# Kernel optimization log

Hardware: AMD Instinct MI355X
Metric: run time of the kernel (lower is better)

## Reference

```python
import jax, jax.numpy as jnp
import numpy as np

H = 23            # hidden size
NUM_LAYERS = 3
F_IN = 32         # input features
OUT = 8           # output size
B = 2048
T = 512


def _gru_dir(x_seq, w_ih, w_hh, b_ih, b_hh, reverse):
    """One direction of a GRU layer. x_seq: [T,B,in] -> [T,B,H] (time-aligned)."""
    # Precompute input-side gates for all timesteps: [T,B,3H]
    xg = jnp.einsum('tbi,gi->tbg', x_seq, w_ih) + b_ih

    def step(h, xg_t):
        hg = h @ w_hh.T + b_hh                      # [B,3H]
        r = jax.nn.sigmoid(xg_t[:, :H] + hg[:, :H])
        z = jax.nn.sigmoid(xg_t[:, H:2 * H] + hg[:, H:2 * H])
        n = jnp.tanh(xg_t[:, 2 * H:] + r * hg[:, 2 * H:])
        h_new = (1.0 - z) * n + z * h
        return h_new, h_new

    h0 = jnp.zeros((x_seq.shape[1], H), x_seq.dtype)
    _, ys = jax.lax.scan(step, h0, xg, reverse=reverse)
    return ys  # outputs aligned to original time order for both directions


def setup_inputs() -> dict:
    key = jax.random.key(0)
    ks = jax.random.split(key, 16)
    s = 1.0 / np.sqrt(H)  # PyTorch GRU default init scale

    def u(k, shape):
        return jax.random.uniform(k, shape, jnp.float32, -s, s)

    inp = {}
    inp['x'] = jax.random.normal(ks[0], (B, T, F_IN), jnp.float32)
    inp['feature_mean'] = jax.random.normal(ks[1], (F_IN,), jnp.float32) * 0.1
    # std in (0.5, 1.5): no zeros, no exact ones
    inp['feature_std'] = jax.random.uniform(ks[2], (F_IN,), jnp.float32, 0.5, 1.5)
    inp['output_mean'] = jax.random.normal(ks[3], (OUT,), jnp.float32) * 0.1
    inp['output_std'] = jax.random.uniform(ks[4], (OUT,), jnp.float32, 0.5, 1.5)

    # layer 0 params, stacked over direction [2, ...]
    inp['w_ih_l0'] = u(ks[5], (2, 3 * H, F_IN))
    inp['w_hh_l0'] = u(ks[6], (2, 3 * H, H))
    inp['b_ih_l0'] = u(ks[7], (2, 3 * H))
    inp['b_hh_l0'] = u(ks[8], (2, 3 * H))
    # layers 1..2, input size = 2H; stacked [layer, dir, ...]
    inp['w_ih_rest'] = u(ks[9], (NUM_LAYERS - 1, 2, 3 * H, 2 * H))
    inp['w_hh_rest'] = u(ks[10], (NUM_LAYERS - 1, 2, 3 * H, H))
    inp['b_ih_rest'] = u(ks[11], (NUM_LAYERS - 1, 2, 3 * H))
    inp['b_hh_rest'] = u(ks[12], (NUM_LAYERS - 1, 2, 3 * H))

    # fc: xavier_uniform for weight, pytorch default uniform for bias
    fan = OUT + 2 * H
    lim = np.sqrt(6.0 / fan)
    inp['fc_w'] = jax.random.uniform(ks[13], (OUT, 2 * H), jnp.float32, -lim, lim)
    bl = 1.0 / np.sqrt(2 * H)
    inp['fc_b'] = jax.random.uniform(ks[14], (OUT,), jnp.float32, -bl, bl)
    return inp


def reference(x, feature_mean, feature_std, output_mean, output_std,
              w_ih_l0, w_hh_l0, b_ih_l0, b_hh_l0,
              w_ih_rest, w_hh_rest, b_ih_rest, b_hh_rest,
              fc_w, fc_b):
    # feature normalization: std==0 -> 1, then zero out features where adjusted std==1
    std_adj = jnp.where(feature_std == 0.0, 1.0, feature_std)
    x = jnp.where(std_adj == 1.0, 0.0, (x - feature_mean) / std_adj)

    seq = jnp.swapaxes(x, 0, 1)  # [T,B,F] for scan over time
    for layer in range(NUM_LAYERS):
        if layer == 0:
            wih, whh, bih, bhh = w_ih_l0, w_hh_l0, b_ih_l0, b_hh_l0
        else:
            wih, whh = w_ih_rest[layer - 1], w_hh_rest[layer - 1]
            bih, bhh = b_ih_rest[layer - 1], b_hh_rest[layer - 1]
        fwd = _gru_dir(seq, wih[0], whh[0], bih[0], bhh[0], reverse=False)
        bwd = _gru_dir(seq, wih[1], whh[1], bih[1], bhh[1], reverse=True)
        seq = jnp.concatenate([fwd, bwd], axis=-1)  # [T,B,2H]

    last = seq[-1]                 # out[:, -1, :] in batch_first layout -> [B,2H]
    out = last @ fc_w.T + fc_b     # [B,OUT]
    out = out * output_std + output_mean
    return out
```

## Files before the change

### kernel.cpp

```cpp
#include <hip/hip_runtime.h>
#include <hip/hip_bf16.h>

constexpr int TT = 512, BB = 2048, NOUT = 8;
constexpr size_t DSTRIDE = (size_t)BB * TT * 24;

typedef __attribute__((ext_vector_type(8))) _Float16 f16x8;
typedef __attribute__((ext_vector_type(4))) float f32x4;
typedef __attribute__((ext_vector_type(2))) _Float16 f16x2;

__device__ __forceinline__ float sigm(float x) {
    float e = __builtin_amdgcn_exp2f(x * -1.4426950408889634f);
    return __builtin_amdgcn_rcpf(1.f + e);
}
__device__ __forceinline__ float tanh_(float x) {
    float e = __builtin_amdgcn_exp2f(x * 2.8853900817779268f);
    return __builtin_fmaf(-2.f, __builtin_amdgcn_rcpf(e + 1.f), 1.f);
}
__device__ __forceinline__ f16x2 asf16x2(unsigned v) {
    f16x2 r; __builtin_memcpy(&r, &v, 4); return r;
}
__device__ __forceinline__ f16x2 pkrtz(float a, float b) {
    auto p = __builtin_amdgcn_cvt_pkrtz(a, b);
    f16x2 r; __builtin_memcpy(&r, &p, 4); return r;
}
__device__ __forceinline__ void wbar() { __builtin_amdgcn_wave_barrier(); }

template <bool L0, bool LAST>
__global__ __launch_bounds__(256) void gru_mfma(
    const void* __restrict__ in_,
    const float* __restrict__ fmean, const float* __restrict__ fstd,
    const float* __restrict__ wih_g, const float* __restrict__ whh_g,
    const float* __restrict__ bih_g, const float* __restrict__ bhh_g,
    unsigned short* __restrict__ outbuf, float* __restrict__ lastbuf)
{
    constexpr int KIN = L0 ? 32 : 46;
    constexpr int KF  = L0 ? 1 : 2;
    constexpr int DSTR = 20;

    __shared__ __align__(16) _Float16  wih_lds[5 * 8 * 16 * 8];
    __shared__ __align__(16) _Float16  whh_h[80 * 24];
    __shared__ __align__(16) float     xg_s[4][2][80 * DSTR];
    __shared__ __align__(16) _Float16  hist_h[4 * 9 * 2 * 32];
    __shared__ float bih_s[80], bhh_s[80];
    __shared__ __align__(16) float an_s[32], cn_s[32];

    const int tid = threadIdx.x, wv = tid >> 6, lane = tid & 63;
    const int bl = lane >> 5, u = lane & 31;
    const int m  = lane & 15, kg = lane >> 4;
    const int dir = blockIdx.y;
    const int bg  = blockIdx.x * 8 + wv * 2 + bl;

    const float* wih_d = wih_g + dir * 69 * KIN;
    const float* whh_d = whh_g + dir * 69 * 23;

    for (int idx = tid; idx < 5120; idx += 256) {
        int t = idx >> 10, r = idx & 1023;
        int kslot = r >> 7, mm = (r >> 3) & 15, j = r & 7;
        int row = t * 16 + mm, k = kslot * 8 + j;
        float v = 0.f;
        if (row < 69) {
            if constexpr (L0) {
                if (k < 32) v = wih_d[row * 32 + k];
            } else {
                if (k < 23) v = wih_d[row * 46 + k];
                else if (k >= 24 && k < 47) v = wih_d[row * 46 + k - 1];
            }
        }
        wih_lds[idx] = (_Float16)v;
    }
    for (int idx = tid; idx < 80 * 24; idx += 256) {
        int j = idx / 24, k = idx - j * 24;
        whh_h[idx] = (j < 69 && k < 23) ? (_Float16)whh_d[j * 23 + k]
                                        : (_Float16)0.f;
    }
    for (int idx = tid; idx < 80; idx += 256) {
        bih_s[idx] = (idx < 69) ? bih_g[dir * 69 + idx] : 0.f;
        bhh_s[idx] = (idx < 69) ? bhh_g[dir * 69 + idx] : 0.f;
    }
    for (int idx = tid; idx < 4 * 9 * 2 * 32; idx += 256)
        hist_h[idx] = (_Float16)0.f;
    if (L0 && tid < 32) {
        float sd = fstd[tid];
        float sa = (sd == 0.f) ? 1.f : sd;
        float a  = (sa == 1.f) ? 0.f : 1.f / sa;
        an_s[tid] = a;
        cn_s[tid] = -fmean[tid] * a;
    }
    __syncthreads();

    unsigned wrp[3][12];
    float bh2;
    #pragma unroll
    for (int r = 0; r < 3; ++r) {
        int row = r * 23 + u;
        #pragma unroll
        for (int k = 0; k < 12; ++k)
            wrp[r][k] = *(const unsigned*)&whh_h[row * 24 + 2 * k];
    }
    bh2 = bhh_s[46 + u];
    float bi5[5];
    #pragma unroll
    for (int t = 0; t < 5; ++t) {
        int n = t * 16 + m;
        bi5[t] = bih_s[n] + (n < 46 ? bhh_s[n] : 0.f);
    }

    const f16x8* bfrag = (const f16x8*)wih_lds;
    f16x8 bfr[5][KF];
    #pragma unroll
    for (int t = 0; t < 5; ++t)
        #pragma unroll
        for (int kf = 0; kf < KF; ++kf)
            bfr[t][kf] = bfrag[(t * 8 + kf * 4 + kg) * 16 + m];

    float an8[L0 ? 8 : 1], cn8[L0 ? 8 : 1];
    if constexpr (L0) {
        #pragma unroll
        for (int j = 0; j < 8; ++j) {
            an8[j] = an_s[kg * 8 + j];
            cn8[j] = cn_s[kg * 8 + j];
        }
    }

    float* db0 = &xg_s[wv][0][0];
    float* db1 = &xg_s[wv][1][0];
    _Float16* hw = &hist_h[wv * 9 * 2 * 32];
    const int ngroups = (LAST && dir == 1) ? 1 : 64;
    float hold = 0.f;

    int sarr[3], cparr[3], ldsoff[3];
    {
        int idx = lane & 31;
        #pragma unroll
        for (int c = 0; c < 3; ++c) {
            int p = idx + 32 * c;
            sarr[c]  = p / 12;
            cparr[c] = p - 12 * sarr[c];
            ldsoff[c] = ((sarr[c] + 1) * 2 + bl) * 32 + 2 * cparr[c];
        }
    }
    unsigned short* dstbase = nullptr;
    if constexpr (!LAST)
        dstbase = outbuf + dir * DSTRIDE + (size_t)bg * TT * 24;

    const int bl_a = m >> 3, tl = m & 7;
    const int b_a  = blockIdx.x * 8 + wv * 2 + bl_a;

    const unsigned short* r0 = (const unsigned short*)in_;
    const unsigned short* r1 = r0 + DSTRIDE;

    float4 xraw0, xraw1;
    f16x8 a0r, a1r;

    {
        const int tg_a = dir ? (511 - tl) : tl;
        if constexpr (L0) {
            const float* xr = (const float*)in_ +
                              ((size_t)b_a * TT + tg_a) * 32 + kg * 8;
            xraw0 = *(const float4*)xr;
            xraw1 = *(const float4*)(xr + 4);
        } else {
            size_t rowoff = ((size_t)b_a * TT + tg_a) * 24;
            const unsigned short* p0 =
                (kg < 3) ? (r0 + rowoff + 8 * kg) : (r1 + rowoff);
            const unsigned short* p1 =
                (kg == 0) ? (r1 + rowoff + 8) : (r1 + rowoff + 16);
            a0r = *(const f16x8*)p0;
            a1r = *(const f16x8*)p1;
        }
    }

    {
        f32x4 acc[5];
        #pragma unroll
        for (int t = 0; t < 5; ++t)
            acc[t] = (f32x4){bi5[t], bi5[t], bi5[t], bi5[t]};
        if constexpr (L0) {
            float xv[8] = {xraw0.x, xraw0.y, xraw0.z, xraw0.w,
                           xraw1.x, xraw1.y, xraw1.z, xraw1.w};
            f16x8 afr;
            #pragma unroll
            for (int j = 0; j < 4; ++j) {
                f16x2 p = pkrtz(xv[2 * j] * an8[2 * j] + cn8[2 * j],
                                xv[2 * j + 1] * an8[2 * j + 1] + cn8[2 * j + 1]);
                afr[2 * j]     = p[0];
                afr[2 * j + 1] = p[1];
            }
            #pragma unroll
            for (int t = 0; t < 5; ++t)
                acc[t] = __builtin_amdgcn_mfma_f32_16x16x32_f16(afr, bfr[t][0],
                                                                acc[t], 0, 0, 0);
        } else {
            f16x8 zz = {};
            f16x8 a0u = a0r;
            f16x8 a1u = (kg >= 2) ? zz : a1r;
            #pragma unroll
            for (int t = 0; t < 5; ++t) {
                acc[t] = __builtin_amdgcn_mfma_f32_16x16x32_f16(a0u, bfr[t][0],
                                                                acc[t], 0, 0, 0);
                acc[t] = __builtin_amdgcn_mfma_f32_16x16x32_f16(a1u, bfr[t][1],
                                                                acc[t], 0, 0, 0);
            }
        }
        #pragma unroll
        for (int t = 0; t < 5; ++t)
            *(f32x4*)&db0[(t * 16 + m) * DSTR + kg * 4] = acc[t];
    }
    if (1 < ngroups) {
        const int tg_a = dir ? (511 - (8 + tl)) : (8 + tl);
        if constexpr (L0) {
            const float* xr = (const float*)in_ +
                              ((size_t)b_a * TT + tg_a) * 32 + kg * 8;
            xraw0 = *(const float4*)xr;
            xraw1 = *(const float4*)(xr + 4);
        } else {
            size_t rowoff = ((size_t)b_a * TT + tg_a) * 24;
            const unsigned short* p0 =
                (kg < 3) ? (r0 + rowoff + 8 * kg) : (r1 + rowoff);
            const unsigned short* p1 =
                (kg == 0) ? (r1 + rowoff + 8) : (r1 + rowoff + 16);
            a0r = *(const f16x8*)p0;
            a1r = *(const f16x8*)p1;
        }
    }

    int cur = 0;
    for (int g = 0; g < ngroups; ++g) {
        float* Dc = cur ? db1 : db0;
        float* Dn = cur ? db0 : db1;
        wbar();

        float xgr[8][3];
        #pragma unroll
        for (int c = 0; c < 3; ++c) {
            const f32x4 lo = *(const f32x4*)&Dc[(c * 23 + u) * DSTR + bl * 8];
            const f32x4 hi = *(const f32x4*)&Dc[(c * 23 + u) * DSTR + bl * 8 + 4];
            #pragma unroll
            for (int s = 0; s < 8; ++s)
                xgr[s][c] = (s < 4) ? lo[s] : hi[s - 4];
        }

        if (g + 1 < ngroups) {
            f32x4 acc[5];
            #pragma unroll
            for (int t = 0; t < 5; ++t)
                acc[t] = (f32x4){bi5[t], bi5[t], bi5[t], bi5[t]};
            if constexpr (L0) {
                float xv[8] = {xraw0.x, xraw0.y, xraw0.z, xraw0.w,
                               xraw1.x, xraw1.y, xraw1.z, xraw1.w};
                f16x8 afr;
                #pragma unroll
                for (int j = 0; j < 4; ++j) {
                    f16x2 p = pkrtz(
                        xv[2 * j] * an8[2 * j] + cn8[2 * j],
                        xv[2 * j + 1] * an8[2 * j + 1] + cn8[2 * j + 1]);
                    afr[2 * j]     = p[0];
                    afr[2 * j + 1] = p[1];
                }
                #pragma unroll
                for (int t = 0; t < 5; ++t)
                    acc[t] = __builtin_amdgcn_mfma_f32_16x16x32_f16(
                        afr, bfr[t][0], acc[t], 0, 0, 0);
            } else {
                f16x8 zz = {};
                f16x8 a0u = a0r;
                f16x8 a1u = (kg >= 2) ? zz : a1r;
                #pragma unroll
                for (int t = 0; t < 5; ++t) {
                    acc[t] = __builtin_amdgcn_mfma_f32_16x16x32_f16(
                        a0u, bfr[t][0], acc[t], 0, 0, 0);
                    acc[t] = __builtin_amdgcn_mfma_f32_16x16x32_f16(
                        a1u, bfr[t][1], acc[t], 0, 0, 0);
                }
            }
            #pragma unroll
            for (int t = 0; t < 5; ++t)
                *(f32x4*)&Dn[(t * 16 + m) * DSTR + kg * 4] = acc[t];

            if (g + 2 < ngroups) {
                const int tg_n = dir ? (511 - ((g + 2) * 8 + tl))
                                     : ((g + 2) * 8 + tl);
                if constexpr (L0) {
                    const float* xr = (const float*)in_ +
                                      ((size_t)b_a * TT + tg_n) * 32 + kg * 8;
                    xraw0 = *(const float4*)xr;
                    xraw1 = *(const float4*)(xr + 4);
                } else {
                    size_t rowoff = ((size_t)b_a * TT + tg_n) * 24;
                    const unsigned short* p0 =
                        (kg < 3) ? (r0 + rowoff + 8 * kg) : (r1 + rowoff);
                    const unsigned short* p1 =
                        (kg == 0) ? (r1 + rowoff + 8) : (r1 + rowoff + 16);
                    a0r = *(const f16x8*)p0;
                    a1r = *(const f16x8*)p1;
                }
            }
        }

        #pragma unroll
        for (int s8 = 0; s8 < 8; ++s8) {
            const _Float16* hr = &hw[(s8 * 2 + bl) * 32];
            uint4 hq0 = *(const uint4*)hr;
            uint4 hq1 = *(const uint4*)(hr + 8);
            uint4 hq2 = *(const uint4*)(hr + 16);
            unsigned hwd[12] = {hq0.x, hq0.y, hq0.z, hq0.w,
                                hq1.x, hq1.y, hq1.z, hq1.w,
                                hq2.x, hq2.y, hq2.z, hq2.w};
            float a0a = xgr[s8][0], a1a = xgr[s8][1], a2a = bh2;
            float a0b = 0.f, a1b = 0.f, a2b = 0.f;
            #pragma unroll
            for (int k = 0; k < 6; ++k) {
                f16x2 hv = asf16x2(hwd[k]);
                a0a = __builtin_amdgcn_fdot2(asf16x2(wrp[0][k]), hv, a0a, false);
                a1a = __builtin_amdgcn_fdot2(asf16x2(wrp[1][k]), hv, a1a, false);
                a2a = __builtin_amdgcn_fdot2(asf16x2(wrp[2][k]), hv, a2a, false);
            }
            #pragma unroll
            for (int k = 6; k < 12; ++k) {
                f16x2 hv = asf16x2(hwd[k]);
                a0b = __builtin_amdgcn_fdot2(asf16x2(wrp[0][k]), hv, a0b, false);
                a1b = __builtin_amdgcn_fdot2(asf16x2(wrp[1][k]), hv, a1b, false);
                a2b = __builtin_amdgcn_fdot2(asf16x2(wrp[2][k]), hv, a2b, false);
            }
            float r_ = sigm(a0a + a0b);
            float z_ = sigm(a1a + a1b);
            float n_ = tanh_(__builtin_fmaf(r_, a2a + a2b, xgr[s8][2]));
            float hnew = n_ + z_ * (hold - n_);
            hold = hnew;
            if constexpr (LAST) {
                int tg = dir ? (511 - (g * 8 + s8)) : (g * 8 + s8);
                if (u < 23 && tg == TT - 1)
                    lastbuf[bg * 48 + dir * 23 + u] = hnew;
            }
            wbar();
            hw[((s8 + 1) * 2 + bl) * 32 + u] = (_Float16)hnew;
            wbar();
        }

        if constexpr (!LAST) {
            #pragma unroll
            for (int c = 0; c < 3; ++c) {
                unsigned w = *(const unsigned*)&hw[ldsoff[c]];
                if (cparr[c] == 11) w &= 0xFFFFu;
                int tg = dir ? (511 - (g * 8 + sarr[c])) : (g * 8 + sarr[c]);
                *(unsigned*)(dstbase + (size_t)tg * 24 + 2 * cparr[c]) = w;
            }
        }
        hw[bl * 32 + u] = (_Float16)hold;
        wbar();
        cur ^= 1;
    }
}

__global__ __launch_bounds__(256) void fc_kernel(
    const float* __restrict__ last, const float* __restrict__ fcw,
    const float* __restrict__ fcb, const float* __restrict__ ostd,
    const float* __restrict__ omean, float* __restrict__ out)
{
    int idx = blockIdx.x * 256 + threadIdx.x;
    if (idx >= BB * NOUT) return;
    int b = idx >> 3, o = idx & 7;
    float acc = fcb[o];
    const float* lr = last + b * 48;
    const float* wr = fcw + o * 46;
    #pragma unroll
    for (int i = 0; i < 46; i++) acc += lr[i] * wr[i];
    out[idx] = acc * ostd[o] + omean[o];
}

extern "C" void kernel_launch(void* const* d_in, const int* in_sizes, int n_in,
                              void* d_out, int out_size, void* d_ws,
                              size_t ws_size, hipStream_t stream)
{
    const float* x     = (const float*)d_in[0];
    const float* fmean = (const float*)d_in[1];
    const float* fstd  = (const float*)d_in[2];
    const float* omean = (const float*)d_in[3];
    const float* ostd  = (const float*)d_in[4];
    const float* wih0  = (const float*)d_in[5];
    const float* whh0  = (const float*)d_in[6];
    const float* bih0  = (const float*)d_in[7];
    const float* bhh0  = (const float*)d_in[8];
    const float* wihr  = (const float*)d_in[9];
    const float* whhr  = (const float*)d_in[10];
    const float* bihr  = (const float*)d_in[11];
    const float* bhhr  = (const float*)d_in[12];
    const float* fcw   = (const float*)d_in[13];
    const float* fcb   = (const float*)d_in[14];

    char* ws = (char*)d_ws;
    const size_t bufBytes = 2 * DSTRIDE * sizeof(unsigned short);
    unsigned short* buf0 = (unsigned short*)ws;
    unsigned short* buf1 = (unsigned short*)(ws + bufBytes);
    float* lastb         = (float*)(ws + 2 * bufBytes);

    dim3 grid(BB / 8, 2);

    gru_mfma<true, false><<<grid, 256, 0, stream>>>(
        x, fmean, fstd, wih0, whh0, bih0, bhh0, buf0, nullptr);
    gru_mfma<false, false><<<grid, 256, 0, stream>>>(
        buf0, nullptr, nullptr, wihr + 0 * 2 * 69 * 46, whhr + 0 * 2 * 69 * 23,
        bihr + 0 * 2 * 69, bhhr + 0 * 2 * 69, buf1, nullptr);
    gru_mfma<false, true><<<grid, 256, 0, stream>>>(
        buf1, nullptr, nullptr, wihr + 1 * 2 * 69 * 46, whhr + 1 * 2 * 69 * 23,
        bihr + 1 * 2 * 69, bhhr + 1 * 2 * 69, nullptr, lastb);
    fc_kernel<<<(BB * NOUT + 255) / 256, 256, 0, stream>>>(lastb, fcw, fcb, ostd,
                                                           omean, (float*)d_out);
}
```

Baseline: 626.0 us.

## Interleave input-projection MFMAs into recurrent steps and drop per-step barriers

The block that computed the next group's input-gate MFMAs, stored them to LDS and prefetched the next inputs used to run before the 8-step recurrence. It is now spread across the recurrent steps: one MFMA tile per step for steps 0–4, the last store at step 5 and the global prefetch at step 6. The goal is to hide that work in the latency of the serial dot/sigmoid/tanh chain. The two wave barriers around each hidden-state LDS write are also removed, leaving a single barrier after the loop. This relies on in-order LDS access within a wave and on the compiler not reordering those accesses, so it risks ordering hazards.

```diff
diff --git a/kernel.cpp b/kernel.cpp
--- a/kernel.cpp
+++ b/kernel.cpp
@@ -240,62 +240,10 @@
                 xgr[s][c] = (s < 4) ? lo[s] : hi[s - 4];
         }
 
-        if (g + 1 < ngroups) {
-            f32x4 acc[5];
-            #pragma unroll
-            for (int t = 0; t < 5; ++t)
-                acc[t] = (f32x4){bi5[t], bi5[t], bi5[t], bi5[t]};
-            if constexpr (L0) {
-                float xv[8] = {xraw0.x, xraw0.y, xraw0.z, xraw0.w,
-                               xraw1.x, xraw1.y, xraw1.z, xraw1.w};
-                f16x8 afr;
-                #pragma unroll
-                for (int j = 0; j < 4; ++j) {
-                    f16x2 p = pkrtz(
-                        xv[2 * j] * an8[2 * j] + cn8[2 * j],
-                        xv[2 * j + 1] * an8[2 * j + 1] + cn8[2 * j + 1]);
-                    afr[2 * j]     = p[0];
-                    afr[2 * j + 1] = p[1];
-                }
-                #pragma unroll
-                for (int t = 0; t < 5; ++t)
-                    acc[t] = __builtin_amdgcn_mfma_f32_16x16x32_f16(
-                        afr, bfr[t][0], acc[t], 0, 0, 0);
-            } else {
-                f16x8 zz = {};
-                f16x8 a0u = a0r;
-                f16x8 a1u = (kg >= 2) ? zz : a1r;
-                #pragma unroll
-                for (int t = 0; t < 5; ++t) {
-                    acc[t] = __builtin_amdgcn_mfma_f32_16x16x32_f16(
-                        a0u, bfr[t][0], acc[t], 0, 0, 0);
-                    acc[t] = __builtin_amdgcn_mfma_f32_16x16x32_f16(
-                        a1u, bfr[t][1], acc[t], 0, 0, 0);
-                }
-            }
-            #pragma unroll
-            for (int t = 0; t < 5; ++t)
-                *(f32x4*)&Dn[(t * 16 + m) * DSTR + kg * 4] = acc[t];
-
-            if (g + 2 < ngroups) {
-                const int tg_n = dir ? (511 - ((g + 2) * 8 + tl))
-                                     : ((g + 2) * 8 + tl);
-                if constexpr (L0) {
-                    const float* xr = (const float*)in_ +
-                                      ((size_t)b_a * TT + tg_n) * 32 + kg * 8;
-                    xraw0 = *(const float4*)xr;
-                    xraw1 = *(const float4*)(xr + 4);
-                } else {
-                    size_t rowoff = ((size_t)b_a * TT + tg_n) * 24;
-                    const unsigned short* p0 =
-                        (kg < 3) ? (r0 + rowoff + 8 * kg) : (r1 + rowoff);
-                    const unsigned short* p1 =
-                        (kg == 0) ? (r1 + rowoff + 8) : (r1 + rowoff + 16);
-                    a0r = *(const f16x8*)p0;
-                    a1r = *(const f16x8*)p1;
-                }
-            }
-        }
+        const bool domfma = (g + 1 < ngroups);
+        const bool doload = (g + 2 < ngroups);
+        f32x4 acc[5];
+        f16x8 a0u, a1u, afr;
 
         #pragma unroll
         for (int s8 = 0; s8 < 8; ++s8) {
@@ -303,6 +251,65 @@
             uint4 hq0 = *(const uint4*)hr;
             uint4 hq1 = *(const uint4*)(hr + 8);
             uint4 hq2 = *(const uint4*)(hr + 16);
+
+            if (s8 <= 4) {
+                if (domfma) {
+                    if constexpr (L0) {
+                        if (s8 == 0) {
+                            float xv[8] = {xraw0.x, xraw0.y, xraw0.z, xraw0.w,
+                                           xraw1.x, xraw1.y, xraw1.z, xraw1.w};
+                            #pragma unroll
+                            for (int j = 0; j < 4; ++j) {
+                                f16x2 p = pkrtz(
+                                    xv[2 * j] * an8[2 * j] + cn8[2 * j],
+                                    xv[2 * j + 1] * an8[2 * j + 1] + cn8[2 * j + 1]);
+                                afr[2 * j]     = p[0];
+                                afr[2 * j + 1] = p[1];
+                            }
+                        }
+                        acc[s8] = (f32x4){bi5[s8], bi5[s8], bi5[s8], bi5[s8]};
+                        acc[s8] = __builtin_amdgcn_mfma_f32_16x16x32_f16(
+                            afr, bfr[s8][0], acc[s8], 0, 0, 0);
+                    } else {
+                        if (s8 == 0) {
+                            f16x8 zz = {};
+                            a0u = a0r;
+                            a1u = (kg >= 2) ? zz : a1r;
+                        }
+                        acc[s8] = (f32x4){bi5[s8], bi5[s8], bi5[s8], bi5[s8]};
+                        acc[s8] = __builtin_amdgcn_mfma_f32_16x16x32_f16(
+                            a0u, bfr[s8][0], acc[s8], 0, 0, 0);
+                        acc[s8] = __builtin_amdgcn_mfma_f32_16x16x32_f16(
+                            a1u, bfr[s8][1], acc[s8], 0, 0, 0);
+                    }
+                    if (s8 >= 1)
+                        *(f32x4*)&Dn[((s8 - 1) * 16 + m) * DSTR + kg * 4] =
+                            acc[s8 - 1];
+                }
+            } else if (s8 == 5) {
+                if (domfma)
+                    *(f32x4*)&Dn[(4 * 16 + m) * DSTR + kg * 4] = acc[4];
+            } else if (s8 == 6) {
+                if (doload) {
+                    const int tg_n = dir ? (511 - ((g + 2) * 8 + tl))
+                                         : ((g + 2) * 8 + tl);
+                    if constexpr (L0) {
+                        const float* xr = (const float*)in_ +
+                                          ((size_t)b_a * TT + tg_n) * 32 + kg * 8;
+                        xraw0 = *(const float4*)xr;
+                        xraw1 = *(const float4*)(xr + 4);
+                    } else {
+                        size_t rowoff = ((size_t)b_a * TT + tg_n) * 24;
+                        const unsigned short* p0 =
+                            (kg < 3) ? (r0 + rowoff + 8 * kg) : (r1 + rowoff);
+                        const unsigned short* p1 =
+                            (kg == 0) ? (r1 + rowoff + 8) : (r1 + rowoff + 16);
+                        a0r = *(const f16x8*)p0;
+                        a1r = *(const f16x8*)p1;
+                    }
+                }
+            }
+
             unsigned hwd[12] = {hq0.x, hq0.y, hq0.z, hq0.w,
                                 hq1.x, hq1.y, hq1.z, hq1.w,
                                 hq2.x, hq2.y, hq2.z, hq2.w};
@@ -332,10 +339,10 @@
                 if (u < 23 && tg == TT - 1)
                     lastbuf[bg * 48 + dir * 23 + u] = hnew;
             }
-            wbar();
             hw[((s8 + 1) * 2 + bl) * 32 + u] = (_Float16)hnew;
-            wbar();
-        }
+        }
+
+        wbar();
 
         if constexpr (!LAST) {
             #pragma unroll
```

Result: no change. 616.6 us (-1.5%).
